# Kernel optimization log

Measured on AMD Instinct MI355X. Metric: run time of the kernel, lower is better.

## Reference

```python
import jax, jax.numpy as jnp
import numpy as np

EPS = 1e-8

def cos_sim(a, b, axis=-1):
    # torch.nn.functional.cosine_similarity: dot / max(|a|*|b|, eps)
    num = jnp.sum(a * b, axis=axis)
    den = jnp.maximum(jnp.linalg.norm(a, axis=axis) * jnp.linalg.norm(b, axis=axis), EPS)
    return num / den

def address_similarity(address, addresses):
    # address: [b, d], addresses: [b, n, d] -> [b, n]
    return cos_sim(address[:, None, :], addresses, axis=2)

def kv_insert(state_k, state_v, k, x, eps=EPS):
    # state_k/state_v: [b, n, d]; k: [b, d]; x: [b, d] (or [1, d], broadcast)
    alpha = cos_sim(k[:, None, :], state_k, axis=2)          # [b, n]
    alpha = jnp.where(alpha > eps, alpha, 0.0)
    return (1.0 - alpha)[..., None] * state_v + alpha[..., None] * x[:, None, :]

def replace(new_value, prev_value, tensr):
    # new_value/prev_value: [b, d]; tensr: [b, n, d]
    sim_to = cos_sim(prev_value[:, None, :], tensr, axis=2)  # [b, n]
    return tensr * (1.0 - sim_to)[..., None] + sim_to[..., None] * new_value[:, None, :]

def select_address(address, addresses, list_of_values):
    cs = address_similarity(address, addresses)              # [b, n]
    return [jnp.sum(values * cs[..., None], axis=1) for values in list_of_values]

def setup_inputs() -> dict:
    key = jax.random.key(0)
    ks = jax.random.split(key, 5)
    B, N, D = 32, 2048, 128
    return {
        "at_addr": jax.random.normal(ks[0], (B, D), dtype=jnp.float32),
        "addresses": jax.random.normal(ks[1], (B, N, D), dtype=jnp.float32),
        "tags": jax.random.normal(ks[2], (B, N, D), dtype=jnp.float32),
        "col1": jax.random.normal(ks[3], (B, N, D), dtype=jnp.float32),
        "col2": jax.random.normal(ks[4], (B, N, D), dtype=jnp.float32),
        "zero_vec": jnp.zeros((D,), dtype=jnp.float32),
        "gc_steps": 2,
    }

def reference(at_addr, addresses, tags, col1, col2, zero_vec, gc_steps):
    B = at_addr.shape[0]
    zv = jnp.broadcast_to(zero_vec[None, :], (B, zero_vec.shape[0]))
    # dereference the App node
    fn_addr, arg_addr = select_address(at_addr, addresses, [col1, col2])
    fn_tag, param_addr, body_addr = select_address(fn_addr, addresses, [tags, col1, col2])
    a_tag, a_l, a_r = select_address(arg_addr, addresses, [tags, col1, col2])
    # substitute arg into param's slot (globally scoped vars)
    tags = kv_insert(addresses, tags, param_addr, a_tag)
    col1 = kv_insert(addresses, col1, param_addr, a_l)
    col2 = kv_insert(addresses, col2, param_addr, a_r)
    col1 = replace(arg_addr, param_addr, col1)
    col2 = replace(arg_addr, param_addr, col2)
    # write the fn body over the App node
    b_tag, b_l, b_r = select_address(body_addr, addresses, [tags, col1, col2])
    tags = kv_insert(addresses, tags, at_addr, b_tag)
    col1 = kv_insert(addresses, col1, at_addr, b_l)
    col2 = kv_insert(addresses, col2, at_addr, b_r)
    # garbage collection
    for _ in range(gc_steps):
        for gaddr in (fn_addr, param_addr, body_addr):
            tags = kv_insert(addresses, tags, gaddr, zv)
            col1 = kv_insert(addresses, col1, gaddr, zv)
            col2 = kv_insert(addresses, col2, gaddr, zv)
    return (tags, col1, col2)
```

## Files before the change

kernel.cpp:

```cpp
#include <hip/hip_runtime.h>

#define EPSF 1e-8f
#define DD 128

struct V2 { float4 A, B; };

__device__ __forceinline__ float4 ld4(const float* p){ return *reinterpret_cast<const float4*>(p); }
__device__ __forceinline__ void st4(float* p, const float4& v){ *reinterpret_cast<float4*>(p) = v; }
__device__ __forceinline__ float dot4(const float4& a, const float4& b){
  return a.x*b.x + a.y*b.y + a.z*b.z + a.w*b.w;
}
__device__ __forceinline__ void fma4(float4& acc, const float4& a, float s){
  acc.x += a.x*s; acc.y += a.y*s; acc.z += a.z*s; acc.w += a.w*s;
}
__device__ __forceinline__ float4 mix4(float a, const float4& v, const float4& x){
  float4 r;
  r.x = (1.f-a)*v.x + a*x.x;
  r.y = (1.f-a)*v.y + a*x.y;
  r.z = (1.f-a)*v.z + a*x.z;
  r.w = (1.f-a)*v.w + a*x.w;
  return r;
}
__device__ __forceinline__ float red16(float v){
  v += __shfl_xor(v, 1);
  v += __shfl_xor(v, 2);
  v += __shfl_xor(v, 4);
  v += __shfl_xor(v, 8);
  return v;
}
__device__ __forceinline__ V2 ldrow(const float* p, size_t base, int l){
  V2 v; v.A = ld4(p + base + l*4); v.B = ld4(p + base + 64 + l*4); return v;
}
__device__ __forceinline__ float dotV(const V2& a, const V2& b){
  return dot4(a.A, b.A) + dot4(a.B, b.B);
}
__device__ __forceinline__ void block_red16(float* red, int g, int l, int t,
                                            const V2& acc, float* dst){
  red[g*DD + l*4+0] = acc.A.x;
  red[g*DD + l*4+1] = acc.A.y;
  red[g*DD + l*4+2] = acc.A.z;
  red[g*DD + l*4+3] = acc.A.w;
  red[g*DD + 64 + l*4+0] = acc.B.x;
  red[g*DD + 64 + l*4+1] = acc.B.y;
  red[g*DD + 64 + l*4+2] = acc.B.z;
  red[g*DD + 64 + l*4+3] = acc.B.w;
  __syncthreads();
  if (t < DD){
    float s = 0.f;
    #pragma unroll
    for (int q = 0; q < 16; ++q) s += red[q*DD + t];
    dst[t] = s;
  }
  __syncthreads();
}

__device__ __forceinline__ void ka_row(const V2& a, const V2& c1, const V2& c2,
                                       const V2& atv, float nat, int l,
                                       float* __restrict__ f2cn, size_t idx,
                                       V2& accF, V2& accA){
  float dp = red16(dotV(atv, a));
  float n2 = red16(dotV(a, a));
  float na = sqrtf(n2);
  float cs = dp / fmaxf(nat * na, EPSF);
  if (l == 0) *reinterpret_cast<float2*>(f2cn + 2*idx) = make_float2(cs, na);
  fma4(accF.A, c1.A, cs); fma4(accF.B, c1.B, cs);
  fma4(accA.A, c2.A, cs); fma4(accA.B, c2.B, cs);
}

__device__ __forceinline__ void kb_row(const V2& a, const V2& t4, const V2& c1, const V2& c2,
                                       const V2& fn, const V2& ag, float nfn, float nag,
                                       float na, int l, float* __restrict__ csfn, size_t idx,
                                       V2& accP, V2& accB, V2& accT, V2& accL, V2& accR){
  float dfn = red16(dotV(fn, a));
  float dag = red16(dotV(ag, a));
  float cf = dfn / fmaxf(nfn*na, EPSF);
  float ca = dag / fmaxf(nag*na, EPSF);
  if (l == 0) csfn[idx] = cf;
  fma4(accP.A, c1.A, cf); fma4(accP.B, c1.B, cf);
  fma4(accB.A, c2.A, cf); fma4(accB.B, c2.B, cf);
  fma4(accT.A, t4.A, ca); fma4(accT.B, t4.B, ca);
  fma4(accL.A, c1.A, ca); fma4(accL.B, c1.B, ca);
  fma4(accR.A, c2.A, ca); fma4(accR.B, c2.B, ca);
}

__device__ __forceinline__ void kc_row(const V2& a, const V2& t4, const V2& c1, const V2& c2,
                                       const V2& ag, const V2& pm, const V2& bd,
                                       const V2& xt, const V2& xl, const V2& xr,
                                       float npm, float nbd, float na, int l,
                                       float* __restrict__ sc4, size_t idx,
                                       V2& accT, V2& accL, V2& accR){
  float dp = red16(dotV(pm, a));
  float db = red16(dotV(bd, a));
  float csp = dp / fmaxf(npm*na, EPSF);
  float ap  = csp > EPSF ? csp : 0.f;
  float csb = db / fmaxf(nbd*na, EPSF);
  V2 tn { mix4(ap, t4.A, xt.A), mix4(ap, t4.B, xt.B) };
  V2 c1n{ mix4(ap, c1.A, xl.A), mix4(ap, c1.B, xl.B) };
  V2 c2n{ mix4(ap, c2.A, xr.A), mix4(ap, c2.B, xr.B) };
  float d1  = red16(dotV(pm, c1n));
  float n21 = red16(dotV(c1n, c1n));
  float d2  = red16(dotV(pm, c2n));
  float n22 = red16(dotV(c2n, c2n));
  float s1 = d1 / fmaxf(npm * sqrtf(n21), EPSF);
  float s2 = d2 / fmaxf(npm * sqrtf(n22), EPSF);
  V2 c1f{ mix4(s1, c1n.A, ag.A), mix4(s1, c1n.B, ag.B) };
  V2 c2f{ mix4(s2, c2n.A, ag.A), mix4(s2, c2n.B, ag.B) };
  if (l == 0) *reinterpret_cast<float4*>(sc4 + 4*idx) = make_float4(ap, csb, s1, s2);
  fma4(accT.A, tn.A,  csb); fma4(accT.B, tn.B,  csb);
  fma4(accL.A, c1f.A, csb); fma4(accL.B, c1f.B, csb);
  fma4(accR.A, c2f.A, csb); fma4(accR.B, c2f.B, csb);
}

__global__ void kFin(const float* __restrict__ part, float* __restrict__ dst,
                     int nvec, int B, int CH){
  int i = blockIdx.x*blockDim.x + threadIdx.x;
  int total = nvec * B * DD;
  if (i >= total) return;
  int d = i & (DD-1);
  int vb = i >> 7;
  const float* p = part + ((size_t)vb*CH)*DD + d;
  float s = 0.f;
  for (int c = 0; c < CH; ++c) s += p[(size_t)c*DD];
  dst[i] = s;
}

__global__ __launch_bounds__(256) void kA(const float* __restrict__ at,
                                          const float* __restrict__ addr,
                                          const float* __restrict__ col1,
                                          const float* __restrict__ col2,
                                          float* __restrict__ f2cn,
                                          float* __restrict__ partA,
                                          int B, int N, int CH){
  __shared__ float red[16*DD];
  int blk = blockIdx.x, b = blk / CH, c = blk % CH;
  int rows = N / CH, n0 = c * rows;
  int t = threadIdx.x, g = t >> 4, l = t & 15;
  size_t bN = (size_t)b * N;

  const float* atp = at + (size_t)b*DD;
  V2 atv{ ld4(atp + l*4), ld4(atp + 64 + l*4) };
  float nat = sqrtf(red16(dotV(atv, atv)));

  V2 zz{ make_float4(0,0,0,0), make_float4(0,0,0,0) };
  V2 accF = zz, accA = zz;
  int r = g;
  #pragma unroll 1
  for (; r + 16 < rows; r += 32){
    size_t n1 = (size_t)n0 + r, n2 = (size_t)n0 + r + 16;
    size_t b1 = (bN + n1)*DD, b2 = (bN + n2)*DD;
    V2 a1 = ldrow(addr, b1, l), a2 = ldrow(addr, b2, l);
    V2 x1 = ldrow(col1, b1, l), x2 = ldrow(col1, b2, l);
    V2 y1 = ldrow(col2, b1, l), y2 = ldrow(col2, b2, l);
    ka_row(a1, x1, y1, atv, nat, l, f2cn, bN + n1, accF, accA);
    ka_row(a2, x2, y2, atv, nat, l, f2cn, bN + n2, accF, accA);
  }
  if (r < rows){
    size_t n1 = (size_t)n0 + r, b1 = (bN + n1)*DD;
    V2 a1 = ldrow(addr, b1, l), x1 = ldrow(col1, b1, l), y1 = ldrow(col2, b1, l);
    ka_row(a1, x1, y1, atv, nat, l, f2cn, bN + n1, accF, accA);
  }
  block_red16(red, g, l, t, accF, partA + ((size_t)(0*B + b)*CH + c)*DD);
  block_red16(red, g, l, t, accA, partA + ((size_t)(1*B + b)*CH + c)*DD);
}

__global__ __launch_bounds__(256) void kB(const float* __restrict__ addr,
                                          const float* __restrict__ tags,
                                          const float* __restrict__ col1,
                                          const float* __restrict__ col2,
                                          const float* __restrict__ f2cn,
                                          float* __restrict__ csfn,
                                          const float* __restrict__ vecs,
                                          float* __restrict__ partB,
                                          int B, int N, int CH){
  __shared__ float red[16*DD];
  int blk = blockIdx.x, b = blk / CH, c = blk % CH;
  int rows = N / CH, n0 = c * rows;
  int t = threadIdx.x, g = t >> 4, l = t & 15;
  size_t bN = (size_t)b * N;
  size_t BDv = (size_t)B * DD;

  const float* fnp = vecs + (size_t)b*DD;
  const float* agp = vecs + BDv + (size_t)b*DD;
  V2 fn{ ld4(fnp + l*4), ld4(fnp + 64 + l*4) };
  V2 ag{ ld4(agp + l*4), ld4(agp + 64 + l*4) };
  float nfn = sqrtf(red16(dotV(fn, fn)));
  float nag = sqrtf(red16(dotV(ag, ag)));

  V2 zz{ make_float4(0,0,0,0), make_float4(0,0,0,0) };
  V2 accP = zz, accB = zz, accT = zz, accL = zz, accR = zz;
  int r = g;
  #pragma unroll 1
  for (; r + 16 < rows; r += 32){
    size_t n1 = (size_t)n0 + r, n2 = (size_t)n0 + r + 16;
    size_t b1 = (bN + n1)*DD, b2 = (bN + n2)*DD;
    V2 a1 = ldrow(addr, b1, l), a2 = ldrow(addr, b2, l);
    V2 t1 = ldrow(tags, b1, l), t2 = ldrow(tags, b2, l);
    V2 x1 = ldrow(col1, b1, l), x2 = ldrow(col1, b2, l);
    V2 y1 = ldrow(col2, b1, l), y2 = ldrow(col2, b2, l);
    float na1 = f2cn[2*(bN + n1) + 1], na2 = f2cn[2*(bN + n2) + 1];
    kb_row(a1, t1, x1, y1, fn, ag, nfn, nag, na1, l, csfn, bN + n1, accP, accB, accT, accL, accR);
    kb_row(a2, t2, x2, y2, fn, ag, nfn, nag, na2, l, csfn, bN + n2, accP, accB, accT, accL, accR);
  }
  if (r < rows){
    size_t n1 = (size_t)n0 + r, b1 = (bN + n1)*DD;
    V2 a1 = ldrow(addr, b1, l), t1 = ldrow(tags, b1, l);
    V2 x1 = ldrow(col1, b1, l), y1 = ldrow(col2, b1, l);
    float na1 = f2cn[2*(bN + n1) + 1];
    kb_row(a1, t1, x1, y1, fn, ag, nfn, nag, na1, l, csfn, bN + n1, accP, accB, accT, accL, accR);
  }
  block_red16(red, g, l, t, accP, partB + ((size_t)(0*B + b)*CH + c)*DD);
  block_red16(red, g, l, t, accB, partB + ((size_t)(1*B + b)*CH + c)*DD);
  block_red16(red, g, l, t, accT, partB + ((size_t)(2*B + b)*CH + c)*DD);
  block_red16(red, g, l, t, accL, partB + ((size_t)(3*B + b)*CH + c)*DD);
  block_red16(red, g, l, t, accR, partB + ((size_t)(4*B + b)*CH + c)*DD);
}

__global__ __launch_bounds__(256) void kC(const float* __restrict__ addr,
                                          const float* __restrict__ tags,
                                          const float* __restrict__ col1,
                                          const float* __restrict__ col2,
                                          const float* __restrict__ f2cn,
                                          float* __restrict__ sc4,
                                          const float* __restrict__ vecs,
                                          float* __restrict__ partC,
                                          int B, int N, int CH){
  __shared__ float red[16*DD];
  int blk = blockIdx.x, b = blk / CH, c = blk % CH;
  int rows = N / CH, n0 = c * rows;
  int t = threadIdx.x, g = t >> 4, l = t & 15;
  size_t bN = (size_t)b * N;
  size_t BDv = (size_t)B * DD;

  const float* vp = vecs + (size_t)b*DD;
  V2 ag{ ld4(vp + 1*BDv + l*4), ld4(vp + 1*BDv + 64 + l*4) };
  V2 pm{ ld4(vp + 2*BDv + l*4), ld4(vp + 2*BDv + 64 + l*4) };
  V2 bd{ ld4(vp + 3*BDv + l*4), ld4(vp + 3*BDv + 64 + l*4) };
  V2 xt{ ld4(vp + 4*BDv + l*4), ld4(vp + 4*BDv + 64 + l*4) };
  V2 xl{ ld4(vp + 5*BDv + l*4), ld4(vp + 5*BDv + 64 + l*4) };
  V2 xr{ ld4(vp + 6*BDv + l*4), ld4(vp + 6*BDv + 64 + l*4) };
  float npm = sqrtf(red16(dotV(pm, pm)));
  float nbd = sqrtf(red16(dotV(bd, bd)));

  V2 zz{ make_float4(0,0,0,0), make_float4(0,0,0,0) };
  V2 accT = zz, accL = zz, accR = zz;
  int r = g;
  #pragma unroll 1
  for (; r + 16 < rows; r += 32){
    size_t n1 = (size_t)n0 + r, n2 = (size_t)n0 + r + 16;
    size_t b1 = (bN + n1)*DD, b2 = (bN + n2)*DD;
    V2 a1 = ldrow(addr, b1, l), a2 = ldrow(addr, b2, l);
    V2 t1 = ldrow(tags, b1, l), t2 = ldrow(tags, b2, l);
    V2 x1 = ldrow(col1, b1, l), x2 = ldrow(col1, b2, l);
    V2 y1 = ldrow(col2, b1, l), y2 = ldrow(col2, b2, l);
    float na1 = f2cn[2*(bN + n1) + 1], na2 = f2cn[2*(bN + n2) + 1];
    kc_row(a1, t1, x1, y1, ag, pm, bd, xt, xl, xr, npm, nbd, na1, l, sc4, bN + n1, accT, accL, accR);
    kc_row(a2, t2, x2, y2, ag, pm, bd, xt, xl, xr, npm, nbd, na2, l, sc4, bN + n2, accT, accL, accR);
  }
  if (r < rows){
    size_t n1 = (size_t)n0 + r, b1 = (bN + n1)*DD;
    V2 a1 = ldrow(addr, b1, l), t1 = ldrow(tags, b1, l);
    V2 x1 = ldrow(col1, b1, l), y1 = ldrow(col2, b1, l);
    float na1 = f2cn[2*(bN + n1) + 1];
    kc_row(a1, t1, x1, y1, ag, pm, bd, xt, xl, xr, npm, nbd, na1, l, sc4, bN + n1, accT, accL, accR);
  }
  block_red16(red, g, l, t, accT, partC + ((size_t)(0*B + b)*CH + c)*DD);
  block_red16(red, g, l, t, accL, partC + ((size_t)(1*B + b)*CH + c)*DD);
  block_red16(red, g, l, t, accR, partC + ((size_t)(2*B + b)*CH + c)*DD);
}

__device__ __forceinline__ void ke_row(size_t bn, int l2, int gcn,
    const float* __restrict__ tags, const float* __restrict__ col1, const float* __restrict__ col2,
    const float* __restrict__ f2cn, const float* __restrict__ csfn, const float* __restrict__ sc4,
    const float4& ag, const float4& xt, const float4& xl, const float4& xr,
    const float4& bt, const float4& bl, const float4& br, const float4& z4,
    float* __restrict__ o_t, float* __restrict__ o_1, float* __restrict__ o_2){
  float4 sc = ld4(sc4 + 4*bn);
  float2 cn = *reinterpret_cast<const float2*>(f2cn + 2*bn);
  float cf = csfn[bn];
  float ap = sc.x, cb = sc.y, s1 = sc.z, s2 = sc.w, c0 = cn.x;
  float aat = c0 > EPSF ? c0 : 0.f;
  float af  = cf > EPSF ? cf : 0.f;
  float ab  = cb > EPSF ? cb : 0.f;
  float q = (1.f-af)*(1.f-ap)*(1.f-ab);
  float P = 1.f;
  for (int k = 0; k < gcn; ++k) P *= q;

  size_t off = bn*DD + (size_t)l2*4;
  float4 t4 = ld4(tags + off), c1 = ld4(col1 + off), c2 = ld4(col2 + off);
  float4 tn  = mix4(ap, t4, xt);
  float4 c1f = mix4(s1, mix4(ap, c1, xl), ag);
  float4 c2f = mix4(s2, mix4(ap, c2, xr), ag);
  float4 u;
  u = mix4(aat, tn, bt);
  u.x = P*u.x + (1.f-P)*z4.x; u.y = P*u.y + (1.f-P)*z4.y;
  u.z = P*u.z + (1.f-P)*z4.z; u.w = P*u.w + (1.f-P)*z4.w;
  st4(o_t + off, u);
  u = mix4(aat, c1f, bl);
  u.x = P*u.x + (1.f-P)*z4.x; u.y = P*u.y + (1.f-P)*z4.y;
  u.z = P*u.z + (1.f-P)*z4.z; u.w = P*u.w + (1.f-P)*z4.w;
  st4(o_1 + off, u);
  u = mix4(aat, c2f, br);
  u.x = P*u.x + (1.f-P)*z4.x; u.y = P*u.y + (1.f-P)*z4.y;
  u.z = P*u.z + (1.f-P)*z4.z; u.w = P*u.w + (1.f-P)*z4.w;
  st4(o_2 + off, u);
}

__global__ __launch_bounds__(256) void kE(const float* __restrict__ tags,
                                          const float* __restrict__ col1,
                                          const float* __restrict__ col2,
                                          float* __restrict__ o_t,
                                          float* __restrict__ o_1,
                                          float* __restrict__ o_2,
                                          const float* __restrict__ f2cn,
                                          const float* __restrict__ csfn,
                                          const float* __restrict__ sc4,
                                          const float* __restrict__ vecs,
                                          const float* __restrict__ zv,
                                          const int* __restrict__ gcp,
                                          int B, int N, int CH){
  int blk = blockIdx.x, b = blk / CH, c = blk % CH;
  int rows = N / CH, n0 = c * rows;
  int t = threadIdx.x;
  int l2 = t & 31, r0 = t >> 5;
  size_t bN = (size_t)b * N;
  size_t BDv = (size_t)B * DD;

  const float* vb = vecs + (size_t)b*DD + (size_t)l2*4;
  float4 ag = ld4(vb + 1*BDv);
  float4 xt = ld4(vb + 4*BDv), xl = ld4(vb + 5*BDv), xr = ld4(vb + 6*BDv);
  float4 bt = ld4(vb + 7*BDv), bl = ld4(vb + 8*BDv), br = ld4(vb + 9*BDv);
  float4 z4 = ld4(zv + l2*4);
  int gcn = gcp[0];

  int r = r0;
  #pragma unroll 1
  for (; r + 8 < rows; r += 16){
    ke_row(bN + n0 + r,     l2, gcn, tags, col1, col2, f2cn, csfn, sc4,
           ag, xt, xl, xr, bt, bl, br, z4, o_t, o_1, o_2);
    ke_row(bN + n0 + r + 8, l2, gcn, tags, col1, col2, f2cn, csfn, sc4,
           ag, xt, xl, xr, bt, bl, br, z4, o_t, o_1, o_2);
  }
  if (r < rows)
    ke_row(bN + n0 + r, l2, gcn, tags, col1, col2, f2cn, csfn, sc4,
           ag, xt, xl, xr, bt, bl, br, z4, o_t, o_1, o_2);
}

extern "C" void kernel_launch(void* const* d_in, const int* in_sizes, int n_in,
                              void* d_out, int out_size, void* d_ws, size_t ws_size,
                              hipStream_t stream){
  const float* at   = (const float*)d_in[0];
  const float* addr = (const float*)d_in[1];
  const float* tags = (const float*)d_in[2];
  const float* col1 = (const float*)d_in[3];
  const float* col2 = (const float*)d_in[4];
  const float* zv   = (const float*)d_in[5];
  const int*   gc   = (const int*)d_in[6];

  int Dd = in_sizes[5];
  int B  = in_sizes[0] / Dd;
  int N  = in_sizes[1] / in_sizes[0];
  (void)Dd;

  size_t S  = (size_t)B * N;
  size_t BD = (size_t)B * DD;

  int CH = 32;
  while (CH > 1){
    size_t need = (7*S + 10*BD + (size_t)10*B*CH*DD) * sizeof(float);
    if (need <= ws_size && (N % CH) == 0) break;
    CH >>= 1;
  }

  float* w = (float*)d_ws;
  float* f2cn  = w;
  float* csfn  = w + 2*S;
  float* sc4   = w + 3*S;
  float* vecs  = w + 7*S;
  float* partA = vecs + 10*BD;
  float* partB = partA + (size_t)2*B*CH*DD;
  float* partC = partB + (size_t)5*B*CH*DD;

  float* o_t = (float*)d_out;
  float* o_1 = o_t + (size_t)B*N*DD;
  float* o_2 = o_1 + (size_t)B*N*DD;

  dim3 blk(256);
  dim3 grid(B*CH);

  kA<<<grid, blk, 0, stream>>>(at, addr, col1, col2, f2cn, partA, B, N, CH);
  kFin<<<(2*B*DD + 255)/256, 256, 0, stream>>>(partA, vecs + 0*BD, 2, B, CH);
  kB<<<grid, blk, 0, stream>>>(addr, tags, col1, col2, f2cn, csfn, vecs, partB, B, N, CH);
  kFin<<<(5*B*DD + 255)/256, 256, 0, stream>>>(partB, vecs + 2*BD, 5, B, CH);
  kC<<<grid, blk, 0, stream>>>(addr, tags, col1, col2, f2cn, sc4, vecs, partC, B, N, CH);
  kFin<<<(3*B*DD + 255)/256, 256, 0, stream>>>(partC, vecs + 7*BD, 3, B, CH);
  kE<<<grid, blk, 0, stream>>>(tags, col1, col2, o_t, o_1, o_2,
                               f2cn, csfn, sc4, vecs, zv, gc, B, N, CH);
}
```

Measured before the change: 126.7 us.

## Fuse the seven-launch pipeline into one cooperative kernel with grid syncs

```diff
diff --git a/kernel.cpp b/kernel.cpp
--- a/kernel.cpp
+++ b/kernel.cpp
@@ -1,4 +1,7 @@
 #include <hip/hip_runtime.h>
+#include <hip/hip_cooperative_groups.h>
+
+namespace cg = cooperative_groups;
 
 #define EPSF 1e-8f
 #define DD 128
@@ -111,163 +114,6 @@
   fma4(accR.A, c2f.A, csb); fma4(accR.B, c2f.B, csb);
 }
 
-__global__ void kFin(const float* __restrict__ part, float* __restrict__ dst,
-                     int nvec, int B, int CH){
-  int i = blockIdx.x*blockDim.x + threadIdx.x;
-  int total = nvec * B * DD;
-  if (i >= total) return;
-  int d = i & (DD-1);
-  int vb = i >> 7;
-  const float* p = part + ((size_t)vb*CH)*DD + d;
-  float s = 0.f;
-  for (int c = 0; c < CH; ++c) s += p[(size_t)c*DD];
-  dst[i] = s;
-}
-
-__global__ __launch_bounds__(256) void kA(const float* __restrict__ at,
-                                          const float* __restrict__ addr,
-                                          const float* __restrict__ col1,
-                                          const float* __restrict__ col2,
-                                          float* __restrict__ f2cn,
-                                          float* __restrict__ partA,
-                                          int B, int N, int CH){
-  __shared__ float red[16*DD];
-  int blk = blockIdx.x, b = blk / CH, c = blk % CH;
-  int rows = N / CH, n0 = c * rows;
-  int t = threadIdx.x, g = t >> 4, l = t & 15;
-  size_t bN = (size_t)b * N;
-
-  const float* atp = at + (size_t)b*DD;
-  V2 atv{ ld4(atp + l*4), ld4(atp + 64 + l*4) };
-  float nat = sqrtf(red16(dotV(atv, atv)));
-
-  V2 zz{ make_float4(0,0,0,0), make_float4(0,0,0,0) };
-  V2 accF = zz, accA = zz;
-  int r = g;
-  #pragma unroll 1
-  for (; r + 16 < rows; r += 32){
-    size_t n1 = (size_t)n0 + r, n2 = (size_t)n0 + r + 16;
-    size_t b1 = (bN + n1)*DD, b2 = (bN + n2)*DD;
-    V2 a1 = ldrow(addr, b1, l), a2 = ldrow(addr, b2, l);
-    V2 x1 = ldrow(col1, b1, l), x2 = ldrow(col1, b2, l);
-    V2 y1 = ldrow(col2, b1, l), y2 = ldrow(col2, b2, l);
-    ka_row(a1, x1, y1, atv, nat, l, f2cn, bN + n1, accF, accA);
-    ka_row(a2, x2, y2, atv, nat, l, f2cn, bN + n2, accF, accA);
-  }
-  if (r < rows){
-    size_t n1 = (size_t)n0 + r, b1 = (bN + n1)*DD;
-    V2 a1 = ldrow(addr, b1, l), x1 = ldrow(col1, b1, l), y1 = ldrow(col2, b1, l);
-    ka_row(a1, x1, y1, atv, nat, l, f2cn, bN + n1, accF, accA);
-  }
-  block_red16(red, g, l, t, accF, partA + ((size_t)(0*B + b)*CH + c)*DD);
-  block_red16(red, g, l, t, accA, partA + ((size_t)(1*B + b)*CH + c)*DD);
-}
-
-__global__ __launch_bounds__(256) void kB(const float* __restrict__ addr,
-                                          const float* __restrict__ tags,
-                                          const float* __restrict__ col1,
-                                          const float* __restrict__ col2,
-                                          const float* __restrict__ f2cn,
-                                          float* __restrict__ csfn,
-                                          const float* __restrict__ vecs,
-                                          float* __restrict__ partB,
-                                          int B, int N, int CH){
-  __shared__ float red[16*DD];
-  int blk = blockIdx.x, b = blk / CH, c = blk % CH;
-  int rows = N / CH, n0 = c * rows;
-  int t = threadIdx.x, g = t >> 4, l = t & 15;
-  size_t bN = (size_t)b * N;
-  size_t BDv = (size_t)B * DD;
-
-  const float* fnp = vecs + (size_t)b*DD;
-  const float* agp = vecs + BDv + (size_t)b*DD;
-  V2 fn{ ld4(fnp + l*4), ld4(fnp + 64 + l*4) };
-  V2 ag{ ld4(agp + l*4), ld4(agp + 64 + l*4) };
-  float nfn = sqrtf(red16(dotV(fn, fn)));
-  float nag = sqrtf(red16(dotV(ag, ag)));
-
-  V2 zz{ make_float4(0,0,0,0), make_float4(0,0,0,0) };
-  V2 accP = zz, accB = zz, accT = zz, accL = zz, accR = zz;
-  int r = g;
-  #pragma unroll 1
-  for (; r + 16 < rows; r += 32){
-    size_t n1 = (size_t)n0 + r, n2 = (size_t)n0 + r + 16;
-    size_t b1 = (bN + n1)*DD, b2 = (bN + n2)*DD;
-    V2 a1 = ldrow(addr, b1, l), a2 = ldrow(addr, b2, l);
-    V2 t1 = ldrow(tags, b1, l), t2 = ldrow(tags, b2, l);
-    V2 x1 = ldrow(col1, b1, l), x2 = ldrow(col1, b2, l);
-    V2 y1 = ldrow(col2, b1, l), y2 = ldrow(col2, b2, l);
-    float na1 = f2cn[2*(bN + n1) + 1], na2 = f2cn[2*(bN + n2) + 1];
-    kb_row(a1, t1, x1, y1, fn, ag, nfn, nag, na1, l, csfn, bN + n1, accP, accB, accT, accL, accR);
-    kb_row(a2, t2, x2, y2, fn, ag, nfn, nag, na2, l, csfn, bN + n2, accP, accB, accT, accL, accR);
-  }
-  if (r < rows){
-    size_t n1 = (size_t)n0 + r, b1 = (bN + n1)*DD;
-    V2 a1 = ldrow(addr, b1, l), t1 = ldrow(tags, b1, l);
-    V2 x1 = ldrow(col1, b1, l), y1 = ldrow(col2, b1, l);
-    float na1 = f2cn[2*(bN + n1) + 1];
-    kb_row(a1, t1, x1, y1, fn, ag, nfn, nag, na1, l, csfn, bN + n1, accP, accB, accT, accL, accR);
-  }
-  block_red16(red, g, l, t, accP, partB + ((size_t)(0*B + b)*CH + c)*DD);
-  block_red16(red, g, l, t, accB, partB + ((size_t)(1*B + b)*CH + c)*DD);
-  block_red16(red, g, l, t, accT, partB + ((size_t)(2*B + b)*CH + c)*DD);
-  block_red16(red, g, l, t, accL, partB + ((size_t)(3*B + b)*CH + c)*DD);
-  block_red16(red, g, l, t, accR, partB + ((size_t)(4*B + b)*CH + c)*DD);
-}
-
-__global__ __launch_bounds__(256) void kC(const float* __restrict__ addr,
-                                          const float* __restrict__ tags,
-                                          const float* __restrict__ col1,
-                                          const float* __restrict__ col2,
-                                          const float* __restrict__ f2cn,
-                                          float* __restrict__ sc4,
-                                          const float* __restrict__ vecs,
-                                          float* __restrict__ partC,
-                                          int B, int N, int CH){
-  __shared__ float red[16*DD];
-  int blk = blockIdx.x, b = blk / CH, c = blk % CH;
-  int rows = N / CH, n0 = c * rows;
-  int t = threadIdx.x, g = t >> 4, l = t & 15;
-  size_t bN = (size_t)b * N;
-  size_t BDv = (size_t)B * DD;
-
-  const float* vp = vecs + (size_t)b*DD;
-  V2 ag{ ld4(vp + 1*BDv + l*4), ld4(vp + 1*BDv + 64 + l*4) };
-  V2 pm{ ld4(vp + 2*BDv + l*4), ld4(vp + 2*BDv + 64 + l*4) };
-  V2 bd{ ld4(vp + 3*BDv + l*4), ld4(vp + 3*BDv + 64 + l*4) };
-  V2 xt{ ld4(vp + 4*BDv + l*4), ld4(vp + 4*BDv + 64 + l*4) };
-  V2 xl{ ld4(vp + 5*BDv + l*4), ld4(vp + 5*BDv + 64 + l*4) };
-  V2 xr{ ld4(vp + 6*BDv + l*4), ld4(vp + 6*BDv + 64 + l*4) };
-  float npm = sqrtf(red16(dotV(pm, pm)));
-  float nbd = sqrtf(red16(dotV(bd, bd)));
-
-  V2 zz{ make_float4(0,0,0,0), make_float4(0,0,0,0) };
-  V2 accT = zz, accL = zz, accR = zz;
-  int r = g;
-  #pragma unroll 1
-  for (; r + 16 < rows; r += 32){
-    size_t n1 = (size_t)n0 + r, n2 = (size_t)n0 + r + 16;
-    size_t b1 = (bN + n1)*DD, b2 = (bN + n2)*DD;
-    V2 a1 = ldrow(addr, b1, l), a2 = ldrow(addr, b2, l);
-    V2 t1 = ldrow(tags, b1, l), t2 = ldrow(tags, b2, l);
-    V2 x1 = ldrow(col1, b1, l), x2 = ldrow(col1, b2, l);
-    V2 y1 = ldrow(col2, b1, l), y2 = ldrow(col2, b2, l);
-    float na1 = f2cn[2*(bN + n1) + 1], na2 = f2cn[2*(bN + n2) + 1];
-    kc_row(a1, t1, x1, y1, ag, pm, bd, xt, xl, xr, npm, nbd, na1, l, sc4, bN + n1, accT, accL, accR);
-    kc_row(a2, t2, x2, y2, ag, pm, bd, xt, xl, xr, npm, nbd, na2, l, sc4, bN + n2, accT, accL, accR);
-  }
-  if (r < rows){
-    size_t n1 = (size_t)n0 + r, b1 = (bN + n1)*DD;
-    V2 a1 = ldrow(addr, b1, l), t1 = ldrow(tags, b1, l);
-    V2 x1 = ldrow(col1, b1, l), y1 = ldrow(col2, b1, l);
-    float na1 = f2cn[2*(bN + n1) + 1];
-    kc_row(a1, t1, x1, y1, ag, pm, bd, xt, xl, xr, npm, nbd, na1, l, sc4, bN + n1, accT, accL, accR);
-  }
-  block_red16(red, g, l, t, accT, partC + ((size_t)(0*B + b)*CH + c)*DD);
-  block_red16(red, g, l, t, accL, partC + ((size_t)(1*B + b)*CH + c)*DD);
-  block_red16(red, g, l, t, accR, partC + ((size_t)(2*B + b)*CH + c)*DD);
-}
-
 __device__ __forceinline__ void ke_row(size_t bn, int l2, int gcn,
     const float* __restrict__ tags, const float* __restrict__ col1, const float* __restrict__ col2,
     const float* __restrict__ f2cn, const float* __restrict__ csfn, const float* __restrict__ sc4,
@@ -303,6 +149,157 @@
   u.x = P*u.x + (1.f-P)*z4.x; u.y = P*u.y + (1.f-P)*z4.y;
   u.z = P*u.z + (1.f-P)*z4.z; u.w = P*u.w + (1.f-P)*z4.w;
   st4(o_2 + off, u);
+}
+
+__global__ void kFin(const float* __restrict__ part, float* __restrict__ dst,
+                     int nvec, int B, int CH){
+  int i = blockIdx.x*blockDim.x + threadIdx.x;
+  int total = nvec * B * DD;
+  if (i >= total) return;
+  int d = i & (DD-1);
+  int vb = i >> 7;
+  const float* p = part + ((size_t)vb*CH)*DD + d;
+  float s = 0.f;
+  for (int c = 0; c < CH; ++c) s += p[(size_t)c*DD];
+  dst[i] = s;
+}
+
+__global__ __launch_bounds__(256) void kA(const float* __restrict__ at,
+                                          const float* __restrict__ addr,
+                                          const float* __restrict__ col1,
+                                          const float* __restrict__ col2,
+                                          float* __restrict__ f2cn,
+                                          float* __restrict__ partA,
+                                          int B, int N, int CH){
+  __shared__ float red[16*DD];
+  int blk = blockIdx.x, b = blk / CH, c = blk % CH;
+  int rows = N / CH, n0 = c * rows;
+  int t = threadIdx.x, g = t >> 4, l = t & 15;
+  size_t bN = (size_t)b * N;
+  const float* atp = at + (size_t)b*DD;
+  V2 atv{ ld4(atp + l*4), ld4(atp + 64 + l*4) };
+  float nat = sqrtf(red16(dotV(atv, atv)));
+  V2 zz{ make_float4(0,0,0,0), make_float4(0,0,0,0) };
+  V2 accF = zz, accA = zz;
+  int r = g;
+  #pragma unroll 1
+  for (; r + 16 < rows; r += 32){
+    size_t n1 = (size_t)n0 + r, n2 = (size_t)n0 + r + 16;
+    size_t b1 = (bN + n1)*DD, b2 = (bN + n2)*DD;
+    V2 a1 = ldrow(addr, b1, l), a2 = ldrow(addr, b2, l);
+    V2 x1 = ldrow(col1, b1, l), x2 = ldrow(col1, b2, l);
+    V2 y1 = ldrow(col2, b1, l), y2 = ldrow(col2, b2, l);
+    ka_row(a1, x1, y1, atv, nat, l, f2cn, bN + n1, accF, accA);
+    ka_row(a2, x2, y2, atv, nat, l, f2cn, bN + n2, accF, accA);
+  }
+  if (r < rows){
+    size_t n1 = (size_t)n0 + r, b1 = (bN + n1)*DD;
+    V2 a1 = ldrow(addr, b1, l), x1 = ldrow(col1, b1, l), y1 = ldrow(col2, b1, l);
+    ka_row(a1, x1, y1, atv, nat, l, f2cn, bN + n1, accF, accA);
+  }
+  block_red16(red, g, l, t, accF, partA + ((size_t)(0*B + b)*CH + c)*DD);
+  block_red16(red, g, l, t, accA, partA + ((size_t)(1*B + b)*CH + c)*DD);
+}
+
+__global__ __launch_bounds__(256) void kB(const float* __restrict__ addr,
+                                          const float* __restrict__ tags,
+                                          const float* __restrict__ col1,
+                                          const float* __restrict__ col2,
+                                          const float* __restrict__ f2cn,
+                                          float* __restrict__ csfn,
+                                          const float* __restrict__ vecs,
+                                          float* __restrict__ partB,
+                                          int B, int N, int CH){
+  __shared__ float red[16*DD];
+  int blk = blockIdx.x, b = blk / CH, c = blk % CH;
+  int rows = N / CH, n0 = c * rows;
+  int t = threadIdx.x, g = t >> 4, l = t & 15;
+  size_t bN = (size_t)b * N;
+  size_t BDv = (size_t)B * DD;
+  const float* fnp = vecs + (size_t)b*DD;
+  const float* agp = vecs + BDv + (size_t)b*DD;
+  V2 fn{ ld4(fnp + l*4), ld4(fnp + 64 + l*4) };
+  V2 ag{ ld4(agp + l*4), ld4(agp + 64 + l*4) };
+  float nfn = sqrtf(red16(dotV(fn, fn)));
+  float nag = sqrtf(red16(dotV(ag, ag)));
+  V2 zz{ make_float4(0,0,0,0), make_float4(0,0,0,0) };
+  V2 accP = zz, accB = zz, accT = zz, accL = zz, accR = zz;
+  int r = g;
+  #pragma unroll 1
+  for (; r + 16 < rows; r += 32){
+    size_t n1 = (size_t)n0 + r, n2 = (size_t)n0 + r + 16;
+    size_t b1 = (bN + n1)*DD, b2 = (bN + n2)*DD;
+    V2 a1 = ldrow(addr, b1, l), a2 = ldrow(addr, b2, l);
+    V2 t1 = ldrow(tags, b1, l), t2 = ldrow(tags, b2, l);
+    V2 x1 = ldrow(col1, b1, l), x2 = ldrow(col1, b2, l);
+    V2 y1 = ldrow(col2, b1, l), y2 = ldrow(col2, b2, l);
+    float na1 = f2cn[2*(bN + n1) + 1], na2 = f2cn[2*(bN + n2) + 1];
+    kb_row(a1, t1, x1, y1, fn, ag, nfn, nag, na1, l, csfn, bN + n1, accP, accB, accT, accL, accR);
+    kb_row(a2, t2, x2, y2, fn, ag, nfn, nag, na2, l, csfn, bN + n2, accP, accB, accT, accL, accR);
+  }
+  if (r < rows){
+    size_t n1 = (size_t)n0 + r, b1 = (bN + n1)*DD;
+    V2 a1 = ldrow(addr, b1, l), t1 = ldrow(tags, b1, l);
+    V2 x1 = ldrow(col1, b1, l), y1 = ldrow(col2, b1, l);
+    float na1 = f2cn[2*(bN + n1) + 1];
+    kb_row(a1, t1, x1, y1, fn, ag, nfn, nag, na1, l, csfn, bN + n1, accP, accB, accT, accL, accR);
+  }
+  block_red16(red, g, l, t, accP, partB + ((size_t)(0*B + b)*CH + c)*DD);
+  block_red16(red, g, l, t, accB, partB + ((size_t)(1*B + b)*CH + c)*DD);
+  block_red16(red, g, l, t, accT, partB + ((size_t)(2*B + b)*CH + c)*DD);
+  block_red16(red, g, l, t, accL, partB + ((size_t)(3*B + b)*CH + c)*DD);
+  block_red16(red, g, l, t, accR, partB + ((size_t)(4*B + b)*CH + c)*DD);
+}
+
+__global__ __launch_bounds__(256) void kC(const float* __restrict__ addr,
+                                          const float* __restrict__ tags,
+                                          const float* __restrict__ col1,
+                                          const float* __restrict__ col2,
+                                          const float* __restrict__ f2cn,
+                                          float* __restrict__ sc4,
+                                          const float* __restrict__ vecs,
+                                          float* __restrict__ partC,
+                                          int B, int N, int CH){
+  __shared__ float red[16*DD];
+  int blk = blockIdx.x, b = blk / CH, c = blk % CH;
+  int rows = N / CH, n0 = c * rows;
+  int t = threadIdx.x, g = t >> 4, l = t & 15;
+  size_t bN = (size_t)b * N;
+  size_t BDv = (size_t)B * DD;
+  const float* vp = vecs + (size_t)b*DD;
+  V2 ag{ ld4(vp + 1*BDv + l*4), ld4(vp + 1*BDv + 64 + l*4) };
+  V2 pm{ ld4(vp + 2*BDv + l*4), ld4(vp + 2*BDv + 64 + l*4) };
+  V2 bd{ ld4(vp + 3*BDv + l*4), ld4(vp + 3*BDv + 64 + l*4) };
+  V2 xt{ ld4(vp + 4*BDv + l*4), ld4(vp + 4*BDv + 64 + l*4) };
+  V2 xl{ ld4(vp + 5*BDv + l*4), ld4(vp + 5*BDv + 64 + l*4) };
+  V2 xr{ ld4(vp + 6*BDv + l*4), ld4(vp + 6*BDv + 64 + l*4) };
+  float npm = sqrtf(red16(dotV(pm, pm)));
+  float nbd = sqrtf(red16(dotV(bd, bd)));
+  V2 zz{ make_float4(0,0,0,0), make_float4(0,0,0,0) };
+  V2 accT = zz, accL = zz, accR = zz;
+  int r = g;
+  #pragma unroll 1
+  for (; r + 16 < rows; r += 32){
+    size_t n1 = (size_t)n0 + r, n2 = (size_t)n0 + r + 16;
+    size_t b1 = (bN + n1)*DD, b2 = (bN + n2)*DD;
+    V2 a1 = ldrow(addr, b1, l), a2 = ldrow(addr, b2, l);
+    V2 t1 = ldrow(tags, b1, l), t2 = ldrow(tags, b2, l);
+    V2 x1 = ldrow(col1, b1, l), x2 = ldrow(col1, b2, l);
+    V2 y1 = ldrow(col2, b1, l), y2 = ldrow(col2, b2, l);
+    float na1 = f2cn[2*(bN + n1) + 1], na2 = f2cn[2*(bN + n2) + 1];
+    kc_row(a1, t1, x1, y1, ag, pm, bd, xt, xl, xr, npm, nbd, na1, l, sc4, bN + n1, accT, accL, accR);
+    kc_row(a2, t2, x2, y2, ag, pm, bd, xt, xl, xr, npm, nbd, na2, l, sc4, bN + n2, accT, accL, accR);
+  }
+  if (r < rows){
+    size_t n1 = (size_t)n0 + r, b1 = (bN + n1)*DD;
+    V2 a1 = ldrow(addr, b1, l), t1 = ldrow(tags, b1, l);
+    V2 x1 = ldrow(col1, b1, l), y1 = ldrow(col2, b1, l);
+    float na1 = f2cn[2*(bN + n1) + 1];
+    kc_row(a1, t1, x1, y1, ag, pm, bd, xt, xl, xr, npm, nbd, na1, l, sc4, bN + n1, accT, accL, accR);
+  }
+  block_red16(red, g, l, t, accT, partC + ((size_t)(0*B + b)*CH + c)*DD);
+  block_red16(red, g, l, t, accL, partC + ((size_t)(1*B + b)*CH + c)*DD);
+  block_red16(red, g, l, t, accR, partC + ((size_t)(2*B + b)*CH + c)*DD);
 }
 
 __global__ __launch_bounds__(256) void kE(const float* __restrict__ tags,
@@ -324,14 +321,12 @@
   int l2 = t & 31, r0 = t >> 5;
   size_t bN = (size_t)b * N;
   size_t BDv = (size_t)B * DD;
-
   const float* vb = vecs + (size_t)b*DD + (size_t)l2*4;
   float4 ag = ld4(vb + 1*BDv);
   float4 xt = ld4(vb + 4*BDv), xl = ld4(vb + 5*BDv), xr = ld4(vb + 6*BDv);
   float4 bt = ld4(vb + 7*BDv), bl = ld4(vb + 8*BDv), br = ld4(vb + 9*BDv);
   float4 z4 = ld4(zv + l2*4);
   int gcn = gcp[0];
-
   int r = r0;
   #pragma unroll 1
   for (; r + 8 < rows; r += 16){
@@ -343,6 +338,191 @@
   if (r < rows)
     ke_row(bN + n0 + r, l2, gcn, tags, col1, col2, f2cn, csfn, sc4,
            ag, xt, xl, xr, bt, bl, br, z4, o_t, o_1, o_2);
+}
+
+__global__ __launch_bounds__(256) void kFused(
+    const float* __restrict__ at,   const float* __restrict__ addr,
+    const float* __restrict__ tags, const float* __restrict__ col1,
+    const float* __restrict__ col2, const float* __restrict__ zv,
+    const int* __restrict__ gcp,
+    float* __restrict__ o_t, float* __restrict__ o_1, float* __restrict__ o_2,
+    float* __restrict__ w, int B, int N, int CH)
+{
+  cg::grid_group grid = cg::this_grid();
+  __shared__ float red[16*DD];
+
+  const size_t S   = (size_t)B * N;
+  const size_t BDv = (size_t)B * DD;
+  float* f2cn  = w;
+  float* csfn  = w + 2*S;
+  float* sc4   = w + 3*S;
+  float* vecs  = w + 7*S;
+  float* partA = vecs + 10*BDv;
+  float* partB = partA + (size_t)2*B*CH*DD;
+  float* partC = partB + (size_t)5*B*CH*DD;
+
+  const int blk = blockIdx.x, b = blk / CH, c = blk % CH;
+  const int rows = N / CH, n0 = c * rows;
+  const int t = threadIdx.x, g = t >> 4, l = t & 15;
+  const size_t bN = (size_t)b * N;
+  const int G = gridDim.x;
+  V2 zz{ make_float4(0,0,0,0), make_float4(0,0,0,0) };
+
+  {
+    const float* atp = at + (size_t)b*DD;
+    V2 atv{ ld4(atp + l*4), ld4(atp + 64 + l*4) };
+    float nat = sqrtf(red16(dotV(atv, atv)));
+    V2 accF = zz, accA = zz;
+    int r = g;
+    #pragma unroll 1
+    for (; r + 16 < rows; r += 32){
+      size_t n1 = (size_t)n0 + r, n2 = (size_t)n0 + r + 16;
+      size_t b1 = (bN + n1)*DD, b2 = (bN + n2)*DD;
+      V2 a1 = ldrow(addr, b1, l), a2 = ldrow(addr, b2, l);
+      V2 x1 = ldrow(col1, b1, l), x2 = ldrow(col1, b2, l);
+      V2 y1 = ldrow(col2, b1, l), y2 = ldrow(col2, b2, l);
+      ka_row(a1, x1, y1, atv, nat, l, f2cn, bN + n1, accF, accA);
+      ka_row(a2, x2, y2, atv, nat, l, f2cn, bN + n2, accF, accA);
+    }
+    if (r < rows){
+      size_t n1 = (size_t)n0 + r, b1 = (bN + n1)*DD;
+      V2 a1 = ldrow(addr, b1, l), x1 = ldrow(col1, b1, l), y1 = ldrow(col2, b1, l);
+      ka_row(a1, x1, y1, atv, nat, l, f2cn, bN + n1, accF, accA);
+    }
+    block_red16(red, g, l, t, accF, partA + ((size_t)(0*B + b)*CH + c)*DD);
+    block_red16(red, g, l, t, accA, partA + ((size_t)(1*B + b)*CH + c)*DD);
+  }
+  grid.sync();
+
+  {
+    int tot = 2*B*DD;
+    for (int i = blk*256 + t; i < tot; i += G*256){
+      int vb = i >> 7, d = i & (DD-1);
+      const float* p = partA + ((size_t)vb*CH)*DD + d;
+      float s = 0.f;
+      for (int cc = 0; cc < CH; ++cc) s += p[(size_t)cc*DD];
+      vecs[i] = s;
+    }
+  }
+  grid.sync();
+
+  {
+    const float* fnp = vecs + (size_t)b*DD;
+    const float* agp = vecs + BDv + (size_t)b*DD;
+    V2 fn{ ld4(fnp + l*4), ld4(fnp + 64 + l*4) };
+    V2 ag{ ld4(agp + l*4), ld4(agp + 64 + l*4) };
+    float nfn = sqrtf(red16(dotV(fn, fn)));
+    float nag = sqrtf(red16(dotV(ag, ag)));
+    V2 accP = zz, accB = zz, accT = zz, accL = zz, accR = zz;
+    int r = g;
+    #pragma unroll 1
+    for (; r + 16 < rows; r += 32){
+      size_t n1 = (size_t)n0 + r, n2 = (size_t)n0 + r + 16;
+      size_t b1 = (bN + n1)*DD, b2 = (bN + n2)*DD;
+      V2 a1 = ldrow(addr, b1, l), a2 = ldrow(addr, b2, l);
+      V2 t1 = ldrow(tags, b1, l), t2 = ldrow(tags, b2, l);
+      V2 x1 = ldrow(col1, b1, l), x2 = ldrow(col1, b2, l);
+      V2 y1 = ldrow(col2, b1, l), y2 = ldrow(col2, b2, l);
+      float na1 = f2cn[2*(bN + n1) + 1], na2 = f2cn[2*(bN + n2) + 1];
+      kb_row(a1, t1, x1, y1, fn, ag, nfn, nag, na1, l, csfn, bN + n1, accP, accB, accT, accL, accR);
+      kb_row(a2, t2, x2, y2, fn, ag, nfn, nag, na2, l, csfn, bN + n2, accP, accB, accT, accL, accR);
+    }
+    if (r < rows){
+      size_t n1 = (size_t)n0 + r, b1 = (bN + n1)*DD;
+      V2 a1 = ldrow(addr, b1, l), t1 = ldrow(tags, b1, l);
+      V2 x1 = ldrow(col1, b1, l), y1 = ldrow(col2, b1, l);
+      float na1 = f2cn[2*(bN + n1) + 1];
+      kb_row(a1, t1, x1, y1, fn, ag, nfn, nag, na1, l, csfn, bN + n1, accP, accB, accT, accL, accR);
+    }
+    block_red16(red, g, l, t, accP, partB + ((size_t)(0*B + b)*CH + c)*DD);
+    block_red16(red, g, l, t, accB, partB + ((size_t)(1*B + b)*CH + c)*DD);
+    block_red16(red, g, l, t, accT, partB + ((size_t)(2*B + b)*CH + c)*DD);
+    block_red16(red, g, l, t, accL, partB + ((size_t)(3*B + b)*CH + c)*DD);
+    block_red16(red, g, l, t, accR, partB + ((size_t)(4*B + b)*CH + c)*DD);
+  }
+  grid.sync();
+
+  {
+    int tot = 5*B*DD;
+    for (int i = blk*256 + t; i < tot; i += G*256){
+      int vb = i >> 7, d = i & (DD-1);
+      const float* p = partB + ((size_t)vb*CH)*DD + d;
+      float s = 0.f;
+      for (int cc = 0; cc < CH; ++cc) s += p[(size_t)cc*DD];
+      vecs[2*BDv + i] = s;
+    }
+  }
+  grid.sync();
+
+  {
+    const float* vp = vecs + (size_t)b*DD;
+    V2 ag{ ld4(vp + 1*BDv + l*4), ld4(vp + 1*BDv + 64 + l*4) };
+    V2 pm{ ld4(vp + 2*BDv + l*4), ld4(vp + 2*BDv + 64 + l*4) };
+    V2 bd{ ld4(vp + 3*BDv + l*4), ld4(vp + 3*BDv + 64 + l*4) };
+    V2 xt{ ld4(vp + 4*BDv + l*4), ld4(vp + 4*BDv + 64 + l*4) };
+    V2 xl{ ld4(vp + 5*BDv + l*4), ld4(vp + 5*BDv + 64 + l*4) };
+    V2 xr{ ld4(vp + 6*BDv + l*4), ld4(vp + 6*BDv + 64 + l*4) };
+    float npm = sqrtf(red16(dotV(pm, pm)));
+    float nbd = sqrtf(red16(dotV(bd, bd)));
+    V2 accT = zz, accL = zz, accR = zz;
+    int r = g;
+    #pragma unroll 1
+    for (; r + 16 < rows; r += 32){
+      size_t n1 = (size_t)n0 + r, n2 = (size_t)n0 + r + 16;
+      size_t b1 = (bN + n1)*DD, b2 = (bN + n2)*DD;
+      V2 a1 = ldrow(addr, b1, l), a2 = ldrow(addr, b2, l);
+      V2 t1 = ldrow(tags, b1, l), t2 = ldrow(tags, b2, l);
+      V2 x1 = ldrow(col1, b1, l), x2 = ldrow(col1, b2, l);
+      V2 y1 = ldrow(col2, b1, l), y2 = ldrow(col2, b2, l);
+      float na1 = f2cn[2*(bN + n1) + 1], na2 = f2cn[2*(bN + n2) + 1];
+      kc_row(a1, t1, x1, y1, ag, pm, bd, xt, xl, xr, npm, nbd, na1, l, sc4, bN + n1, accT, accL, accR);
+      kc_row(a2, t2, x2, y2, ag, pm, bd, xt, xl, xr, npm, nbd, na2, l, sc4, bN + n2, accT, accL, accR);
+    }
+    if (r < rows){
+      size_t n1 = (size_t)n0 + r, b1 = (bN + n1)*DD;
+      V2 a1 = ldrow(addr, b1, l), t1 = ldrow(tags, b1, l);
+      V2 x1 = ldrow(col1, b1, l), y1 = ldrow(col2, b1, l);
+      float na1 = f2cn[2*(bN + n1) + 1];
+      kc_row(a1, t1, x1, y1, ag, pm, bd, xt, xl, xr, npm, nbd, na1, l, sc4, bN + n1, accT, accL, accR);
+    }
+    block_red16(red, g, l, t, accT, partC + ((size_t)(0*B + b)*CH + c)*DD);
+    block_red16(red, g, l, t, accL, partC + ((size_t)(1*B + b)*CH + c)*DD);
+    block_red16(red, g, l, t, accR, partC + ((size_t)(2*B + b)*CH + c)*DD);
+  }
+  grid.sync();
+
+  {
+    int tot = 3*B*DD;
+    for (int i = blk*256 + t; i < tot; i += G*256){
+      int vb = i >> 7, d = i & (DD-1);
+      const float* p = partC + ((size_t)vb*CH)*DD + d;
+      float s = 0.f;
+      for (int cc = 0; cc < CH; ++cc) s += p[(size_t)cc*DD];
+      vecs[7*BDv + i] = s;
+    }
+  }
+  grid.sync();
+
+  {
+    const int l2 = t & 31, r0 = t >> 5;
+    const float* vb = vecs + (size_t)b*DD + (size_t)l2*4;
+    float4 ag = ld4(vb + 1*BDv);
+    float4 xt = ld4(vb + 4*BDv), xl = ld4(vb + 5*BDv), xr = ld4(vb + 6*BDv);
+    float4 bt = ld4(vb + 7*BDv), bl = ld4(vb + 8*BDv), br = ld4(vb + 9*BDv);
+    float4 z4 = ld4(zv + l2*4);
+    int gcn = gcp[0];
+    int r = r0;
+    #pragma unroll 1
+    for (; r + 8 < rows; r += 16){
+      ke_row(bN + n0 + r,     l2, gcn, tags, col1, col2, f2cn, csfn, sc4,
+             ag, xt, xl, xr, bt, bl, br, z4, o_t, o_1, o_2);
+      ke_row(bN + n0 + r + 8, l2, gcn, tags, col1, col2, f2cn, csfn, sc4,
+             ag, xt, xl, xr, bt, bl, br, z4, o_t, o_1, o_2);
+    }
+    if (r < rows)
+      ke_row(bN + n0 + r, l2, gcn, tags, col1, col2, f2cn, csfn, sc4,
+             ag, xt, xl, xr, bt, bl, br, z4, o_t, o_1, o_2);
+  }
 }
 
 extern "C" void kernel_launch(void* const* d_in, const int* in_sizes, int n_in,
@@ -364,12 +544,19 @@
   size_t S  = (size_t)B * N;
   size_t BD = (size_t)B * DD;
 
+  int maxB = 0;
+  if (hipOccupancyMaxActiveBlocksPerMultiprocessor(&maxB, kFused, 256, 0) != hipSuccess || maxB < 1)
+    maxB = 0;
+  long cap = (long)maxB * 256;
+
   int CH = 32;
   while (CH > 1){
     size_t need = (7*S + 10*BD + (size_t)10*B*CH*DD) * sizeof(float);
     if (need <= ws_size && (N % CH) == 0) break;
     CH >>= 1;
   }
+  int CHc = CH;
+  while (CHc > 1 && (long)B*CHc > cap) CHc >>= 1;
 
   float* w = (float*)d_ws;
   float* f2cn  = w;
@@ -384,15 +571,26 @@
   float* o_1 = o_t + (size_t)B*N*DD;
   float* o_2 = o_1 + (size_t)B*N*DD;
 
-  dim3 blk(256);
-  dim3 grid(B*CH);
-
-  kA<<<grid, blk, 0, stream>>>(at, addr, col1, col2, f2cn, partA, B, N, CH);
-  kFin<<<(2*B*DD + 255)/256, 256, 0, stream>>>(partA, vecs + 0*BD, 2, B, CH);
-  kB<<<grid, blk, 0, stream>>>(addr, tags, col1, col2, f2cn, csfn, vecs, partB, B, N, CH);
-  kFin<<<(5*B*DD + 255)/256, 256, 0, stream>>>(partB, vecs + 2*BD, 5, B, CH);
-  kC<<<grid, blk, 0, stream>>>(addr, tags, col1, col2, f2cn, sc4, vecs, partC, B, N, CH);
-  kFin<<<(3*B*DD + 255)/256, 256, 0, stream>>>(partC, vecs + 7*BD, 3, B, CH);
-  kE<<<grid, blk, 0, stream>>>(tags, col1, col2, o_t, o_1, o_2,
-                               f2cn, csfn, sc4, vecs, zv, gc, B, N, CH);
-}
+  bool done = false;
+  if (cap >= (long)B*CHc && CHc >= 8){
+    int G = B * CHc;
+    void* args[] = {(void*)&at, (void*)&addr, (void*)&tags, (void*)&col1, (void*)&col2,
+                    (void*)&zv, (void*)&gc, (void*)&o_t, (void*)&o_1, (void*)&o_2,
+                    (void*)&w, (void*)&B, (void*)&N, (void*)&CHc};
+    hipError_t err = hipLaunchCooperativeKernel((const void*)kFused, dim3(G), dim3(256),
+                                                args, 0, stream);
+    done = (err == hipSuccess);
+  }
+  if (!done){
+    dim3 blk(256);
+    dim3 grid(B*CH);
+    kA<<<grid, blk, 0, stream>>>(at, addr, col1, col2, f2cn, partA, B, N, CH);
+    kFin<<<(2*B*DD + 255)/256, 256, 0, stream>>>(partA, vecs + 0*BD, 2, B, CH);
+    kB<<<grid, blk, 0, stream>>>(addr, tags, col1, col2, f2cn, csfn, vecs, partB, B, N, CH);
+    kFin<<<(5*B*DD + 255)/256, 256, 0, stream>>>(partB, vecs + 2*BD, 5, B, CH);
+    kC<<<grid, blk, 0, stream>>>(addr, tags, col1, col2, f2cn, sc4, vecs, partC, B, N, CH);
+    kFin<<<(3*B*DD + 255)/256, 256, 0, stream>>>(partC, vecs + 7*BD, 3, B, CH);
+    kE<<<grid, blk, 0, stream>>>(tags, col1, col2, o_t, o_1, o_2,
+                                 f2cn, csfn, sc4, vecs, zv, gc, B, N, CH);
+  }
+}
```

After: 273.0 us. +115.5%, slower.
